# Optimization experiments

Hardware: AMD Instinct MI355X
Metric: run time of the kernel (lower is better)

Reference implementation:

```python
import jax, jax.numpy as jnp
import numpy as np
from jax import lax

B, N, DDESC = 8, 256, 128
COST_KP = 1.0
COST_DESC = 1.0
BLOCK = 128  # row block for L1 cdist


def setup_inputs() -> dict:
    key = jax.random.key(0)
    k1, k2, k3, k4, k5 = jax.random.split(key, 5)
    W, H = 640, 480
    wh = jnp.array([W, H], jnp.float32)
    kp1 = jax.random.uniform(k1, (B, N, 2)) * wh          # pixel coords
    kp2 = jax.random.uniform(k2, (B, N, 2)) * wh
    desc1 = jax.random.normal(k3, (B, N, DDESC))
    desc2 = jax.random.normal(k4, (B, N, DDESC))
    theta = jax.random.uniform(k5, (1,)) * (2.0 * jnp.pi)
    return {
        "theta": theta,
        "my_feature": jnp.concatenate([kp1, desc1], -1),
        "my_tf_feature": jnp.concatenate([kp2, desc2], -1),
        "my_width": W,
        "my_height": H,
    }


def _fundamental_8point(p1, p2):
    """Normalized 8-point algorithm (cv2.FM_8POINT): p2^T F p1 = 0, F[2,2]=1."""
    def norm(p):
        m = p.mean(0)
        d = jnp.sqrt(((p - m) ** 2).sum(1)).mean()
        s = jnp.sqrt(2.0) / d
        T = jnp.array([[1.0, 0.0, 0.0], [0.0, 1.0, 0.0], [0.0, 0.0, 0.0]]) * s \
            + jnp.zeros((3, 3)).at[0, 2].set(-s * m[0]).at[1, 2].set(-s * m[1]).at[2, 2].set(1.0)
        return (p - m) * s, T
    x1, T1 = norm(p1)
    x2, T2 = norm(p2)
    u1, v1 = x1[:, 0], x1[:, 1]
    u2, v2 = x2[:, 0], x2[:, 1]
    A = jnp.stack([u2 * u1, u2 * v1, u2, v2 * u1, v2 * v1, v2, u1, v1, jnp.ones_like(u1)], 1)
    _, _, Vt = jnp.linalg.svd(A, full_matrices=False)      # Vt: [9,9]
    Fm = Vt[-1].reshape(3, 3)
    U, S, Vt2 = jnp.linalg.svd(Fm)
    Fm = (U * S.at[2].set(0.0)) @ Vt2                      # enforce rank 2
    Fm = T2.T @ Fm @ T1
    return Fm / Fm[2, 2]


def _cdist_l1(a, b):
    """torch.cdist(p=1) without materializing [M,M,D]; blocked over rows."""
    M, D = a.shape
    ab = a.reshape(M // BLOCK, BLOCK, D)
    rows = lax.map(lambda blk: jnp.abs(blk[:, None, :] - b[None, :, :]).sum(-1), ab)
    return rows.reshape(M, b.shape[0])


def _cost_matrix(theta, my_feature, my_tf_feature, W, H):
    my_kp = my_feature[..., :2]
    my_tf_kp = my_tf_feature[..., :2]
    my_desc = my_feature[..., 2:]
    my_tf_desc = my_tf_feature[..., 2:]

    c, s = jnp.cos(theta[0]), jnp.sin(theta[0])
    zero = jnp.zeros(())
    one = jnp.ones(())
    Tm = jnp.stack([
        jnp.stack([c, -s, zero, zero]),
        jnp.stack([s, c, zero, zero]),
        jnp.stack([zero, zero, one, zero]),
        jnp.stack([zero, zero, zero, one]),
    ])  # make_transformation_M(theta, 0, 0): z-rotation, no translation

    # homogeneous image-centered coords: [B, 4, N]
    all_kp = jnp.stack([
        my_kp[:, :, 0] - 0.5 * W,
        -my_kp[:, :, 1] + 0.5 * H,
        jnp.zeros_like(my_kp[:, :, 0]),
        jnp.ones_like(my_kp[:, :, 0]),
    ], 1)
    cal = jnp.round(jnp.einsum('ij,bjn->bin', Tm, all_kp))[:, :2, :]  # [B,2,N]
    g = cal.transpose(0, 2, 1)                                        # [B,N,2]
    o = jnp.stack([g[..., 0] + 0.5 * W, -g[..., 1] + 0.5 * H], -1)    # back to pixels

    pts1 = my_tf_kp.astype(jnp.int32).reshape(B * N, 2).astype(jnp.float32)
    pts2 = o.astype(jnp.int32).reshape(B * N, 2).astype(jnp.float32)
    F = _fundamental_8point(pts1, pts2)

    ones = jnp.ones((B * N, 1), jnp.float32)
    p1h = jnp.concatenate([pts1, ones], 1)
    p2h = jnp.concatenate([pts2, ones], 1)
    cost_kp = jnp.abs((p1h @ F.astype(jnp.float32)) @ p2h.T)          # [BN, BN]

    cost_desc = _cdist_l1(my_desc.reshape(B * N, -1), my_tf_desc.reshape(B * N, -1))
    C = COST_KP * cost_kp + COST_DESC * cost_desc
    return C.reshape(B, N, B * N)


def _hungarian_np(cost):
    """scipy.optimize.linear_sum_assignment (JV shortest augmenting path), numpy."""
    cost = np.asarray(cost, dtype=np.float64)
    n = cost.shape[0]
    u = np.zeros(n)
    v = np.zeros(n)
    path = np.full(n, -1, dtype=np.int64)
    col4row = np.full(n, -1, dtype=np.int64)
    row4col = np.full(n, -1, dtype=np.int64)
    for cur_row in range(n):
        shortest = np.full(n, np.inf)
        remaining = np.ones(n, dtype=bool)
        SR = []
        i = cur_row
        min_val = 0.0
        sink = -1
        while sink == -1:
            SR.append(i)
            idx = np.nonzero(remaining)[0]
            r = min_val + cost[i, idx] - u[i] - v[idx]
            better = r < shortest[idx]
            bidx = idx[better]
            shortest[bidx] = r[better]
            path[bidx] = i
            jpos = idx[np.argmin(shortest[idx])]
            min_val = shortest[jpos]
            remaining[jpos] = False
            if row4col[jpos] == -1:
                sink = jpos
            else:
                i = row4col[jpos]
        u[cur_row] += min_val
        for i2 in SR:
            if i2 != cur_row:
                u[i2] += min_val - shortest[col4row[i2]]
        scanned = ~remaining
        v[scanned] -= min_val - shortest[scanned]
        j = sink
        while True:
            i2 = path[j]
            row4col[j] = i2
            col4row[i2], j = j, col4row[i2]
            if i2 == cur_row:
                break
    return col4row


def reference(theta, my_feature, my_tf_feature, my_width, my_height):
    C = _cost_matrix(theta, my_feature, my_tf_feature, float(my_width), float(my_height))
    Cn = np.asarray(jax.device_get(C))
    # diagonal [N,N] blocks: C.split(num_kp, -1) -> c[i] in the torch code
    cols = np.stack([_hungarian_np(Cn[i, :, i * N:(i + 1) * N]) for i in range(B)])
    rows = np.tile(np.arange(N), (B, 1))
    matches = jnp.asarray(np.stack([rows, cols], 1), dtype=jnp.int32)  # [B,2,N]
    return C, matches
```

## Files before the change

### kernel.cpp

```cpp
#include <hip/hip_runtime.h>
#include <hip/hip_bf16.h>
#include <cfloat>
#include <math.h>

#define BB 8
#define NN 256
#define BN 2048
#define DD 128
#define FEAT 130

__global__ __launch_bounds__(256) void prep_kernel(
    const float* __restrict__ theta,
    const float* __restrict__ feat1,
    const float* __restrict__ feat2,
    const int* __restrict__ wp, const int* __restrict__ hp,
    float* __restrict__ pts1, float* __restrict__ pts2) {
  int i = blockIdx.x * 256 + threadIdx.x;
  if (i >= BN) return;
  double W = (double)wp[0], H = (double)hp[0];
  double th = (double)theta[0];
  double c = cos(th), s = sin(th);
  double kx = (double)feat1[(size_t)i * FEAT + 0];
  double ky = (double)feat1[(size_t)i * FEAT + 1];
  double x = kx - 0.5 * W;
  double y = -ky + 0.5 * H;
  double calx = rint(c * x - s * y);
  double caly = rint(s * x + c * y);
  double ox = calx + 0.5 * W;
  double oy = -caly + 0.5 * H;
  pts2[2 * i]     = (float)(int)ox;
  pts2[2 * i + 1] = (float)(int)oy;
  pts1[2 * i]     = (float)(int)feat2[(size_t)i * FEAT + 0];
  pts1[2 * i + 1] = (float)(int)feat2[(size_t)i * FEAT + 1];
}

__device__ inline double wred(double x) {
#pragma unroll
  for (int off = 32; off > 0; off >>= 1) x += __shfl_down(x, off, 64);
  return x;
}

#define JROT(P, Q) {                                                          \
  double app_ = __shfl(Bc[P], P);                                             \
  double aqq_ = __shfl(Bc[Q], Q);                                             \
  double apq_ = __shfl(Bc[P], Q);                                             \
  double c_, s_;                                                              \
  if (fabs(apq_) > 1e-300) {                                                  \
    double tau_ = (aqq_ - app_) / (2.0 * apq_);                               \
    double t_ = (tau_ >= 0.0 ? 1.0 : -1.0) / (fabs(tau_) + sqrt(1.0 + tau_ * tau_)); \
    c_ = 1.0 / sqrt(1.0 + t_ * t_);                                           \
    s_ = t_ * c_;                                                             \
  } else { c_ = 1.0; s_ = 0.0; }                                              \
  const int prt_ = (jln == P) ? Q : ((jln == Q) ? P : jln);                   \
  const bool isP_ = (jln == P), isQ_ = (jln == Q);                            \
  _Pragma("unroll")                                                           \
  for (int ii = 0; ii < 9; ++ii) {                                            \
    double ob_ = __shfl(Bc[ii], prt_);                                        \
    double ov_ = __shfl(Vc[ii], prt_);                                        \
    if (isP_) { Bc[ii] = c_ * Bc[ii] - s_ * ob_; Vc[ii] = c_ * Vc[ii] - s_ * ov_; } \
    if (isQ_) { Bc[ii] = s_ * ob_ + c_ * Bc[ii]; Vc[ii] = s_ * ov_ + c_ * Vc[ii]; } \
  }                                                                           \
  { double rp_ = Bc[P], rq_ = Bc[Q];                                          \
    Bc[P] = c_ * rp_ - s_ * rq_; Bc[Q] = s_ * rp_ + c_ * rq_; } }

#define ROT3(P, Q) {                                                          \
  double apq_ = A3[P][Q];                                                     \
  double c_, s_;                                                              \
  if (fabs(apq_) > 1e-300) {                                                  \
    double tau_ = (A3[Q][Q] - A3[P][P]) / (2.0 * apq_);                       \
    double t_ = (tau_ >= 0.0 ? 1.0 : -1.0) / (fabs(tau_) + sqrt(1.0 + tau_ * tau_)); \
    c_ = 1.0 / sqrt(1.0 + t_ * t_); s_ = t_ * c_;                             \
  } else { c_ = 1.0; s_ = 0.0; }                                              \
  _Pragma("unroll")                                                           \
  for (int ii = 0; ii < 3; ++ii) { double a_ = A3[ii][P], b_ = A3[ii][Q];     \
    A3[ii][P] = c_ * a_ - s_ * b_; A3[ii][Q] = s_ * a_ + c_ * b_; }           \
  _Pragma("unroll")                                                           \
  for (int ii = 0; ii < 3; ++ii) { double a_ = A3[P][ii], b_ = A3[Q][ii];     \
    A3[P][ii] = c_ * a_ - s_ * b_; A3[Q][ii] = s_ * a_ + c_ * b_; }           \
  _Pragma("unroll")                                                           \
  for (int ii = 0; ii < 3; ++ii) { double a_ = V3[ii][P], b_ = V3[ii][Q];     \
    V3[ii][P] = c_ * a_ - s_ * b_; V3[ii][Q] = s_ * a_ + c_ * b_; } }

__global__ __launch_bounds__(256) void fmat_kernel(
    const float* __restrict__ pts1f, const float* __restrict__ pts2f,
    double* __restrict__ Fout) {
  __shared__ double sred[6];
  __shared__ double sATA[45];
  __shared__ double sV[9][16];
  __shared__ double sEv[16];
  const int tid = threadIdx.x;
  const int lane = tid & 63;
  if (tid < 6) sred[tid] = 0.0;
  if (tid < 45) sATA[tid] = 0.0;
  __syncthreads();

  double sx1 = 0, sy1 = 0, sx2 = 0, sy2 = 0;
  for (int p = tid; p < BN; p += 256) {
    sx1 += (double)pts1f[2 * p];     sy1 += (double)pts1f[2 * p + 1];
    sx2 += (double)pts2f[2 * p];     sy2 += (double)pts2f[2 * p + 1];
  }
  sx1 = wred(sx1); sy1 = wred(sy1); sx2 = wred(sx2); sy2 = wred(sy2);
  if (lane == 0) {
    atomicAdd(&sred[0], sx1); atomicAdd(&sred[1], sy1);
    atomicAdd(&sred[2], sx2); atomicAdd(&sred[3], sy2);
  }
  __syncthreads();
  const double m1x = sred[0] * (1.0 / BN), m1y = sred[1] * (1.0 / BN);
  const double m2x = sred[2] * (1.0 / BN), m2y = sred[3] * (1.0 / BN);

  double d1 = 0, d2 = 0;
  for (int p = tid; p < BN; p += 256) {
    double ax = (double)pts1f[2 * p] - m1x, ay = (double)pts1f[2 * p + 1] - m1y;
    double bx = (double)pts2f[2 * p] - m2x, by = (double)pts2f[2 * p + 1] - m2y;
    d1 += sqrt(ax * ax + ay * ay);
    d2 += sqrt(bx * bx + by * by);
  }
  d1 = wred(d1); d2 = wred(d2);
  if (lane == 0) { atomicAdd(&sred[4], d1); atomicAdd(&sred[5], d2); }
  __syncthreads();
  const double s1 = sqrt(2.0) / (sred[4] * (1.0 / BN));
  const double s2 = sqrt(2.0) / (sred[5] * (1.0 / BN));

  double acc45[45];
#pragma unroll
  for (int e = 0; e < 45; ++e) acc45[e] = 0.0;
  for (int p = tid; p < BN; p += 256) {
    double u1 = ((double)pts1f[2 * p]     - m1x) * s1;
    double v1 = ((double)pts1f[2 * p + 1] - m1y) * s1;
    double u2 = ((double)pts2f[2 * p]     - m2x) * s2;
    double v2 = ((double)pts2f[2 * p + 1] - m2y) * s2;
    double r[9] = {u2 * u1, u2 * v1, u2, v2 * u1, v2 * v1, v2, u1, v1, 1.0};
#pragma unroll
    for (int a = 0; a < 9; ++a)
#pragma unroll
      for (int b = a; b < 9; ++b)
        acc45[9 * a - (a * (a - 1)) / 2 + (b - a)] += r[a] * r[b];
  }
#pragma unroll
  for (int e = 0; e < 45; ++e) {
    double vv = wred(acc45[e]);
    if (lane == 0) atomicAdd(&sATA[e], vv);
  }
  __syncthreads();

  if (tid < 64) {
    const int jln = tid;
    double Bc[9], Vc[9];
#pragma unroll
    for (int i2 = 0; i2 < 9; ++i2) {
      if (jln < 9) {
        int a = i2 < jln ? i2 : jln;
        int b = i2 < jln ? jln : i2;
        Bc[i2] = sATA[9 * a - (a * (a - 1)) / 2 + (b - a)];
      } else Bc[i2] = 0.0;
      Vc[i2] = (i2 == jln) ? 1.0 : 0.0;
    }
    for (int sw = 0; sw < 7; ++sw) {
      JROT(0,1) JROT(0,2) JROT(0,3) JROT(0,4) JROT(0,5) JROT(0,6) JROT(0,7) JROT(0,8)
      JROT(1,2) JROT(1,3) JROT(1,4) JROT(1,5) JROT(1,6) JROT(1,7) JROT(1,8)
      JROT(2,3) JROT(2,4) JROT(2,5) JROT(2,6) JROT(2,7) JROT(2,8)
      JROT(3,4) JROT(3,5) JROT(3,6) JROT(3,7) JROT(3,8)
      JROT(4,5) JROT(4,6) JROT(4,7) JROT(4,8)
      JROT(5,6) JROT(5,7) JROT(5,8)
      JROT(6,7) JROT(6,8)
      JROT(7,8)
    }
    double ev = 0.0;
#pragma unroll
    for (int i2 = 0; i2 < 9; ++i2) if (jln == i2) ev = Bc[i2];
    if (jln < 9) {
      sEv[jln] = ev;
#pragma unroll
      for (int i2 = 0; i2 < 9; ++i2) sV[i2][jln] = Vc[i2];
    }
  }
  __syncthreads();

  if (tid == 0) {
    int jm = 0; double be = sEv[0];
#pragma unroll
    for (int jj = 1; jj < 9; ++jj) if (sEv[jj] < be) { be = sEv[jj]; jm = jj; }
    double F0[9];
#pragma unroll
    for (int i2 = 0; i2 < 9; ++i2) F0[i2] = sV[i2][jm];
    double M00 = F0[0], M01 = F0[1], M02 = F0[2];
    double M10 = F0[3], M11 = F0[4], M12 = F0[5];
    double M20 = F0[6], M21 = F0[7], M22 = F0[8];
    double A3[3][3], V3[3][3];
    A3[0][0] = M00*M00 + M10*M10 + M20*M20;
    A3[0][1] = M00*M01 + M10*M11 + M20*M21;
    A3[0][2] = M00*M02 + M10*M12 + M20*M22;
    A3[1][1] = M01*M01 + M11*M11 + M21*M21;
    A3[1][2] = M01*M02 + M11*M12 + M21*M22;
    A3[2][2] = M02*M02 + M12*M12 + M22*M22;
    A3[1][0] = A3[0][1]; A3[2][0] = A3[0][2]; A3[2][1] = A3[1][2];
#pragma unroll
    for (int ii = 0; ii < 3; ++ii)
#pragma unroll
      for (int jj = 0; jj < 3; ++jj) V3[ii][jj] = (ii == jj) ? 1.0 : 0.0;
    for (int sw = 0; sw < 10; ++sw) { ROT3(0,1) ROT3(0,2) ROT3(1,2) }
    double w0 = A3[0][0], w1 = A3[1][1], w2 = A3[2][2];
    double vx, vy, vz;
    if (w0 <= w1 && w0 <= w2)      { vx = V3[0][0]; vy = V3[1][0]; vz = V3[2][0]; }
    else if (w1 <= w2)             { vx = V3[0][1]; vy = V3[1][1]; vz = V3[2][1]; }
    else                           { vx = V3[0][2]; vy = V3[1][2]; vz = V3[2][2]; }
    double Mv0 = M00 * vx + M01 * vy + M02 * vz;
    double Mv1 = M10 * vx + M11 * vy + M12 * vz;
    double Mv2 = M20 * vx + M21 * vy + M22 * vz;
    double F200 = M00 - Mv0 * vx, F201 = M01 - Mv0 * vy, F202 = M02 - Mv0 * vz;
    double F210 = M10 - Mv1 * vx, F211 = M11 - Mv1 * vy, F212 = M12 - Mv1 * vz;
    double F220 = M20 - Mv2 * vx, F221 = M21 - Mv2 * vy, F222 = M22 - Mv2 * vz;
    double R00 = s2 * F200, R01 = s2 * F201, R02 = s2 * F202;
    double R10 = s2 * F210, R11 = s2 * F211, R12 = s2 * F212;
    double R20 = -s2 * m2x * F200 - s2 * m2y * F210 + F220;
    double R21 = -s2 * m2x * F201 - s2 * m2y * F211 + F221;
    double R22 = -s2 * m2x * F202 - s2 * m2y * F212 + F222;
    double D00 = s1 * R00, D10 = s1 * R10, D20 = s1 * R20;
    double D01 = s1 * R01, D11 = s1 * R11, D21 = s1 * R21;
    double D02 = -s1 * m1x * R00 - s1 * m1y * R01 + R02;
    double D12 = -s1 * m1x * R10 - s1 * m1y * R11 + R12;
    double D22 = -s1 * m1x * R20 - s1 * m1y * R21 + R22;
    Fout[0] = D00 / D22; Fout[1] = D01 / D22; Fout[2] = D02 / D22;
    Fout[3] = D10 / D22; Fout[4] = D11 / D22; Fout[5] = D12 / D22;
    Fout[6] = D20 / D22; Fout[7] = D21 / D22; Fout[8] = D22 / D22;
  }
}

__global__ __launch_bounds__(256) void cost_kernel(
    const float* __restrict__ feat1,
    const float* __restrict__ feat2,
    const float* __restrict__ pts1,
    const float* __restrict__ pts2,
    const double* __restrict__ Fd,
    float* __restrict__ Cout) {
  __shared__ float D1[128][68];
  __shared__ float D2[128][68];
  __shared__ float a0s[64], a1s[64], a2s[64], p2xs[64], p2ys[64];
  const int tid = threadIdx.x;
  const int rowbase = blockIdx.y * 64;
  const int colbase = blockIdx.x * 64;
#pragma unroll
  for (int it = 0; it < 32; ++it) {
    int idx = it * 256 + tid;
    int r = idx >> 7, k = idx & 127;
    D1[k][r] = feat1[(size_t)(rowbase + r) * FEAT + 2 + k];
    D2[k][r] = feat2[(size_t)(colbase + r) * FEAT + 2 + k];
  }
  if (tid < 64) {
    float x1 = pts1[2 * (rowbase + tid)], y1 = pts1[2 * (rowbase + tid) + 1];
    a0s[tid] = (float)(Fd[0] * x1 + Fd[3] * y1 + Fd[6]);
    a1s[tid] = (float)(Fd[1] * x1 + Fd[4] * y1 + Fd[7]);
    a2s[tid] = (float)(Fd[2] * x1 + Fd[5] * y1 + Fd[8]);
    p2xs[tid] = pts2[2 * (colbase + tid)];
    p2ys[tid] = pts2[2 * (colbase + tid) + 1];
  }
  __syncthreads();
  const int tx = tid & 15, ty = tid >> 4;
  float acc[4][4] = {};
#pragma unroll 4
  for (int k = 0; k < 128; ++k) {
    float4 av = *(const float4*)&D1[k][ty * 4];
    float4 bv = *(const float4*)&D2[k][tx * 4];
    float ar[4] = {av.x, av.y, av.z, av.w};
    float br[4] = {bv.x, bv.y, bv.z, bv.w};
#pragma unroll
    for (int r = 0; r < 4; ++r)
#pragma unroll
      for (int c = 0; c < 4; ++c)
        acc[r][c] += fabsf(ar[r] - br[c]);
  }
#pragma unroll
  for (int r = 0; r < 4; ++r) {
    int row = rowbase + ty * 4 + r;
    float a0 = a0s[ty * 4 + r], a1 = a1s[ty * 4 + r], a2 = a2s[ty * 4 + r];
    float4 o;
    float* op = &o.x;
#pragma unroll
    for (int c = 0; c < 4; ++c) {
      float kp = fabsf(a0 * p2xs[tx * 4 + c] + a1 * p2ys[tx * 4 + c] + a2);
      op[c] = acc[r][c] + kp;
    }
    *(float4*)&Cout[(size_t)row * BN + colbase + tx * 4] = o;
  }
}

#define NROWS_C 152

__device__ __forceinline__ unsigned long long sortkey(double d) {
  long long b = __double_as_longlong(d);
  long long m = (b >> 63) | (long long)0x8000000000000000LL;
  return (unsigned long long)(b ^ m);
}

template<int CTRL>
__device__ __forceinline__ unsigned dpprm32(unsigned x) {
  int y = __builtin_amdgcn_update_dpp(0, (int)x, CTRL, 0xF, 0xF, true);
  unsigned u = (unsigned)y;
  return u < x ? u : x;
}
template<int CTRL>
__device__ __forceinline__ unsigned long long dpprm64(unsigned long long x) {
  int lo = (int)(unsigned)x, hi = (int)(unsigned)(x >> 32);
  int lo2 = __builtin_amdgcn_update_dpp(0, lo, CTRL, 0xF, 0xF, true);
  int hi2 = __builtin_amdgcn_update_dpp(0, hi, CTRL, 0xF, 0xF, true);
  unsigned long long y =
      ((unsigned long long)(unsigned)hi2 << 32) | (unsigned)lo2;
  return y < x ? y : x;
}

__device__ __forceinline__ unsigned wave_min_u32(unsigned x) {
  unsigned h = dpprm32<0x121>(x);
  h = dpprm32<0x122>(h);
  h = dpprm32<0x124>(h);
  h = dpprm32<0x128>(h);
  unsigned g0 = (unsigned)__builtin_amdgcn_readlane((int)h, 0);
  unsigned g1 = (unsigned)__builtin_amdgcn_readlane((int)h, 16);
  unsigned g2 = (unsigned)__builtin_amdgcn_readlane((int)h, 32);
  unsigned g3 = (unsigned)__builtin_amdgcn_readlane((int)h, 48);
  unsigned ga = g0 < g1 ? g0 : g1, gb = g2 < g3 ? g2 : g3;
  return ga < gb ? ga : gb;
}

__device__ __forceinline__ double rl64(double x, int l) {
  long long bb = __double_as_longlong(x);
  int lo = __builtin_amdgcn_readlane((int)(bb & 0xFFFFFFFFLL), l);
  int hi = __builtin_amdgcn_readlane((int)(bb >> 32), l);
  return __longlong_as_double(((long long)hi << 32) | (unsigned)lo);
}
__device__ __forceinline__ unsigned long long rdpair(unsigned ghi, unsigned glo, int l) {
  return ((unsigned long long)(unsigned)__builtin_amdgcn_readlane((int)ghi, l) << 32)
       | (unsigned)__builtin_amdgcn_readlane((int)glo, l);
}

#define UPD(K, CK, KK, SH, PP) {                                       \
  double d_ = (base + (double)(CK)) - v##K;                            \
  bool a_ = ((rem >> (K)) & 1u) && (d_ < (SH));                        \
  (SH) = a_ ? d_ : (SH);                                               \
  (KK) = a_ ? sortkey(d_) : (KK);                                      \
  (PP) = a_ ? i : (PP); }

#define ROWLOAD(I) ((I) < NROWS_C ? *(const float4*)&rcache[(I)][lane * 4]   \
                                  : *(const float4*)(Cb + (size_t)(I) * BN + lane * 4))

#define R4C_OF(LI) ((LI) == 0 ? r4c0 : (LI) == 1 ? r4c1 : (LI) == 2 ? r4c2 : r4c3)
#define U4_OF(LI)  ((LI) == 0 ? u40  : (LI) == 1 ? u41  : (LI) == 2 ? u42  : u43)
#define SH_OF(LI)  ((LI) == 0 ? sh0  : (LI) == 1 ? sh1  : (LI) == 2 ? sh2  : sh3)

__global__ __launch_bounds__(64) void hungarian_kernel(
    const float* __restrict__ C, float* __restrict__ out_matches) {
  const int b = blockIdx.x;
  const int lane = threadIdx.x;
  __shared__ float rcache[NROWS_C][NN];
  __shared__ int c4r_lds[NN];
  __shared__ double u_sd[NN];
  __shared__ int flist[NN];
  const float* Cb = C + (size_t)b * NN * BN + (size_t)b * NN;

  for (int t = lane; t < NROWS_C * (NN / 4); t += 64) {
    int r = t >> 6, q = t & 63;
    *(float4*)&rcache[r][q * 4] = *(const float4*)(Cb + (size_t)r * BN + q * 4);
  }
  for (int r = lane; r < NN; r += 64) c4r_lds[r] = -1;
  __syncthreads();

  for (int i = 0; i < NN; ++i) {
    float4 cr = ROWLOAD(i);
    float m01 = fminf(cr.x, cr.y), m23 = fminf(cr.z, cr.w);
    unsigned gm = wave_min_u32(__float_as_uint(fminf(m01, m23)));
    if (lane == 0) u_sd[i] = (double)__uint_as_float(gm);
  }
  __syncthreads();

  double v0, v1, v2, v3;
  int am0 = 0, am1 = 0, am2 = 0, am3 = 0;
  {
    double c0 = DBL_MAX, c1 = DBL_MAX, c2 = DBL_MAX, c3 = DBL_MAX;
    for (int i = 0; i < NN; ++i) {
      float4 cr = ROWLOAD(i);
      double uu = u_sd[i];
      double s0 = (double)cr.x - uu; if (s0 < c0) { c0 = s0; am0 = i; }
      double s1 = (double)cr.y - uu; if (s1 < c1) { c1 = s1; am1 = i; }
      double s2 = (double)cr.z - uu; if (s2 < c2) { c2 = s2; am2 = i; }
      double s3 = (double)cr.w - uu; if (s3 < c3) { c3 = s3; am3 = i; }
    }
    v0 = c0; v1 = c1; v2 = c2; v3 = c3;
  }

  int r4c0, r4c1, r4c2, r4c3;
  { int old = atomicCAS(&c4r_lds[am0], -1, lane * 4 + 0); r4c0 = (old == -1) ? am0 : -1; }
  { int old = atomicCAS(&c4r_lds[am1], -1, lane * 4 + 1); r4c1 = (old == -1) ? am1 : -1; }
  { int old = atomicCAS(&c4r_lds[am2], -1, lane * 4 + 2); r4c2 = (old == -1) ? am2 : -1; }
  { int old = atomicCAS(&c4r_lds[am3], -1, lane * 4 + 3); r4c3 = (old == -1) ? am3 : -1; }
  __syncthreads();
  int c4r0 = c4r_lds[lane * 4 + 0];
  int c4r1 = c4r_lds[lane * 4 + 1];
  int c4r2 = c4r_lds[lane * 4 + 2];
  int c4r3 = c4r_lds[lane * 4 + 3];
  double u40 = (r4c0 >= 0) ? u_sd[r4c0] : 0.0;
  double u41 = (r4c1 >= 0) ? u_sd[r4c1] : 0.0;
  double u42 = (r4c2 >= 0) ? u_sd[r4c2] : 0.0;
  double u43 = (r4c3 >= 0) ? u_sd[r4c3] : 0.0;

  int totfree = 0;
  for (int r0 = 0; r0 < NN; r0 += 64) {
    bool fr = (c4r_lds[r0 + lane] < 0);
    unsigned long long mask = __ballot(fr);
    int idx = totfree + __builtin_popcountll(mask & ((1ULL << lane) - 1ULL));
    if (fr) flist[idx] = r0 + lane;
    totfree += (int)__builtin_popcountll(mask);
  }
  __syncthreads();

  const unsigned long long KMAX = 0xFFFFFFFFFFFFFFFFULL;

  for (int fi = 0; fi < totfree; ++fi) {
    const int cur = flist[fi];
    unsigned long long k0 = KMAX, k1 = KMAX, k2 = KMAX, k3 = KMAX;
    double sh0 = DBL_MAX, sh1 = DBL_MAX, sh2 = DBL_MAX, sh3 = DBL_MAX;
    int p0 = -1, p1 = -1, p2 = -1, p3 = -1;
    unsigned rem = 0xFu;
    double minval = 0.0;
    const double ucur0 = u_sd[cur];
    double ui = ucur0;
    int i = cur;
    int sink = -1;
    float4 cr = ROWLOAD(cur);
    while (true) {
      double base = minval - ui;
      UPD(0, cr.x, k0, sh0, p0)
      UPD(1, cr.y, k1, sh1, p1)
      UPD(2, cr.z, k2, sh2, p2)
      UPD(3, cr.w, k3, sh3, p3)
      unsigned long long m01 = k0 < k1 ? k0 : k1;
      unsigned long long m23 = k2 < k3 ? k2 : k3;
      unsigned long long kl = m01 < m23 ? m01 : m23;
      int myli = (k0 == kl) ? 0 : (k1 == kl) ? 1 : (k2 == kl) ? 2 : 3;
      double mysh = SH_OF(myli);
      double myu  = U4_OF(myli);
      int myrc    = R4C_OF(myli);
      unsigned packed = ((unsigned)(myrc + 1) & 0xFFFFu) | ((unsigned)myli << 16);
      unsigned hi = (unsigned)(kl >> 32);
      unsigned mh = wave_min_u32(hi);
      unsigned long long bal = __ballot(hi == mh);
      int wl;
      if (__builtin_popcountll(bal) == 1) {
        wl = (int)__builtin_ctzll(bal);
      } else {
        unsigned long long gg = dpprm64<0x121>(kl);
        gg = dpprm64<0x122>(gg); gg = dpprm64<0x124>(gg); gg = dpprm64<0x128>(gg);
        unsigned glo2 = (unsigned)gg, ghi2 = (unsigned)(gg >> 32);
        unsigned long long r0 = rdpair(ghi2, glo2, 0);
        unsigned long long r1 = rdpair(ghi2, glo2, 16);
        unsigned long long r2 = rdpair(ghi2, glo2, 32);
        unsigned long long r3 = rdpair(ghi2, glo2, 48);
        unsigned long long ra = r0 < r1 ? r0 : r1, rb = r2 < r3 ? r2 : r3;
        unsigned long long g = ra < rb ? ra : rb;
        bal = __ballot(kl == g);
        wl = (int)__builtin_ctzll(bal);
      }
      int pk = __builtin_amdgcn_readlane((int)packed, wl);
      minval = rl64(mysh, wl);
      double uin = rl64(myu, wl);
      int rc = (pk & 0xFFFF) - 1;
      int li = pk >> 16;
      float4 nxt;
      if (rc >= 0) nxt = ROWLOAD(rc);
      if (lane == wl) {
        if (myli == 0)      k0 = KMAX;
        else if (myli == 1) k1 = KMAX;
        else if (myli == 2) k2 = KMAX;
        else                k3 = KMAX;
        rem &= ~(1u << myli);
      }
      if (rc < 0) { sink = wl * 4 + li; break; }
      ui = uin;
      i = rc;
      cr = nxt;
    }
    if (!(rem & 1u)) { double dl = minval - sh0; v0 -= dl; if (r4c0 >= 0) u40 += dl; }
    if (!(rem & 2u)) { double dl = minval - sh1; v1 -= dl; if (r4c1 >= 0) u41 += dl; }
    if (!(rem & 4u)) { double dl = minval - sh2; v2 -= dl; if (r4c2 >= 0) u42 += dl; }
    if (!(rem & 8u)) { double dl = minval - sh3; v3 -= dl; if (r4c3 >= 0) u43 += dl; }
    int j = sink;
    while (true) {
      int slot = j & 3, ow = j >> 2;
      int myp = (slot == 0) ? p0 : (slot == 1) ? p1 : (slot == 2) ? p2 : p3;
      int i2 = __builtin_amdgcn_readlane(myp, ow);
      int s2 = i2 & 3, ow2 = i2 >> 2;
      int myc = (s2 == 0) ? c4r0 : (s2 == 1) ? c4r1 : (s2 == 2) ? c4r2 : c4r3;
      int jn = __builtin_amdgcn_readlane(myc, ow2);
      double newu;
      if (i2 == cur) {
        newu = ucur0 + minval;
      } else {
        int slj = jn & 3, owj = jn >> 2;
        double myuj = (slj == 0) ? u40 : (slj == 1) ? u41
                    : (slj == 2) ? u42 : u43;
        newu = rl64(myuj, owj);
      }
      if (lane == ow) {
        if (slot == 0) { r4c0 = i2; u40 = newu; }
        else if (slot == 1) { r4c1 = i2; u41 = newu; }
        else if (slot == 2) { r4c2 = i2; u42 = newu; }
        else { r4c3 = i2; u43 = newu; }
      }
      if (lane == ow2) {
        if (s2 == 0) c4r0 = j; else if (s2 == 1) c4r1 = j;
        else if (s2 == 2) c4r2 = j; else c4r3 = j;
      }
      if (i2 == cur) break;
      j = jn;
    }
  }

  float4 ridx, cidx;
  ridx.x = (float)(lane * 4 + 0); ridx.y = (float)(lane * 4 + 1);
  ridx.z = (float)(lane * 4 + 2); ridx.w = (float)(lane * 4 + 3);
  cidx.x = (float)c4r0; cidx.y = (float)c4r1;
  cidx.z = (float)c4r2; cidx.w = (float)c4r3;
  *(float4*)&out_matches[b * 2 * NN + lane * 4] = ridx;
  *(float4*)&out_matches[b * 2 * NN + NN + lane * 4] = cidx;
}

extern "C" void kernel_launch(void* const* d_in, const int* in_sizes, int n_in,
                              void* d_out, int out_size, void* d_ws, size_t ws_size,
                              hipStream_t stream) {
  const float* theta = (const float*)d_in[0];
  const float* feat1 = (const float*)d_in[1];
  const float* feat2 = (const float*)d_in[2];
  const int* wp = (const int*)d_in[3];
  const int* hp = (const int*)d_in[4];
  float* out = (float*)d_out;

  float* pts1 = (float*)d_ws;
  float* pts2 = pts1 + 2 * BN;
  double* Fd = (double*)(pts2 + 2 * BN);

  prep_kernel<<<BN / 256, 256, 0, stream>>>(theta, feat1, feat2, wp, hp, pts1, pts2);
  fmat_kernel<<<1, 256, 0, stream>>>(pts1, pts2, Fd);
  dim3 grid(BN / 64, BN / 64);
  cost_kernel<<<grid, 256, 0, stream>>>(feat1, feat2, pts1, pts2, Fd, out);
  hungarian_kernel<<<BB, 64, 0, stream>>>(out, out + (size_t)BN * BN);
}
```

Baseline: 1.733 ms.

## Fuse prep into fmat kernel, cut Jacobi sweeps, simplify Hungarian min keys

```diff
diff --git a/kernel.cpp b/kernel.cpp
--- a/kernel.cpp
+++ b/kernel.cpp
@@ -8,31 +8,6 @@
 #define BN 2048
 #define DD 128
 #define FEAT 130
-
-__global__ __launch_bounds__(256) void prep_kernel(
-    const float* __restrict__ theta,
-    const float* __restrict__ feat1,
-    const float* __restrict__ feat2,
-    const int* __restrict__ wp, const int* __restrict__ hp,
-    float* __restrict__ pts1, float* __restrict__ pts2) {
-  int i = blockIdx.x * 256 + threadIdx.x;
-  if (i >= BN) return;
-  double W = (double)wp[0], H = (double)hp[0];
-  double th = (double)theta[0];
-  double c = cos(th), s = sin(th);
-  double kx = (double)feat1[(size_t)i * FEAT + 0];
-  double ky = (double)feat1[(size_t)i * FEAT + 1];
-  double x = kx - 0.5 * W;
-  double y = -ky + 0.5 * H;
-  double calx = rint(c * x - s * y);
-  double caly = rint(s * x + c * y);
-  double ox = calx + 0.5 * W;
-  double oy = -caly + 0.5 * H;
-  pts2[2 * i]     = (float)(int)ox;
-  pts2[2 * i + 1] = (float)(int)oy;
-  pts1[2 * i]     = (float)(int)feat2[(size_t)i * FEAT + 0];
-  pts1[2 * i + 1] = (float)(int)feat2[(size_t)i * FEAT + 1];
-}
 
 __device__ inline double wred(double x) {
 #pragma unroll
@@ -82,7 +57,11 @@
     V3[ii][P] = c_ * a_ - s_ * b_; V3[ii][Q] = s_ * a_ + c_ * b_; } }
 
 __global__ __launch_bounds__(256) void fmat_kernel(
-    const float* __restrict__ pts1f, const float* __restrict__ pts2f,
+    const float* __restrict__ theta,
+    const float* __restrict__ feat1,
+    const float* __restrict__ feat2,
+    const int* __restrict__ wp, const int* __restrict__ hp,
+    float* pts1f, float* pts2f,
     double* __restrict__ Fout) {
   __shared__ double sred[6];
   __shared__ double sATA[45];
@@ -92,6 +71,26 @@
   const int lane = tid & 63;
   if (tid < 6) sred[tid] = 0.0;
   if (tid < 45) sATA[tid] = 0.0;
+
+  {
+    double W = (double)wp[0], H = (double)hp[0];
+    double th = (double)theta[0];
+    double c = cos(th), s = sin(th);
+    for (int i = tid; i < BN; i += 256) {
+      double kx = (double)feat1[(size_t)i * FEAT + 0];
+      double ky = (double)feat1[(size_t)i * FEAT + 1];
+      double x = kx - 0.5 * W;
+      double y = -ky + 0.5 * H;
+      double calx = rint(c * x - s * y);
+      double caly = rint(s * x + c * y);
+      double ox = calx + 0.5 * W;
+      double oy = -caly + 0.5 * H;
+      pts2f[2 * i]     = (float)(int)ox;
+      pts2f[2 * i + 1] = (float)(int)oy;
+      pts1f[2 * i]     = (float)(int)feat2[(size_t)i * FEAT + 0];
+      pts1f[2 * i + 1] = (float)(int)feat2[(size_t)i * FEAT + 1];
+    }
+  }
   __syncthreads();
 
   double sx1 = 0, sy1 = 0, sx2 = 0, sy2 = 0;
@@ -155,7 +154,7 @@
       } else Bc[i2] = 0.0;
       Vc[i2] = (i2 == jln) ? 1.0 : 0.0;
     }
-    for (int sw = 0; sw < 7; ++sw) {
+    for (int sw = 0; sw < 5; ++sw) {
       JROT(0,1) JROT(0,2) JROT(0,3) JROT(0,4) JROT(0,5) JROT(0,6) JROT(0,7) JROT(0,8)
       JROT(1,2) JROT(1,3) JROT(1,4) JROT(1,5) JROT(1,6) JROT(1,7) JROT(1,8)
       JROT(2,3) JROT(2,4) JROT(2,5) JROT(2,6) JROT(2,7) JROT(2,8)
@@ -284,13 +283,7 @@
   }
 }
 
-#define NROWS_C 152
-
-__device__ __forceinline__ unsigned long long sortkey(double d) {
-  long long b = __double_as_longlong(d);
-  long long m = (b >> 63) | (long long)0x8000000000000000LL;
-  return (unsigned long long)(b ^ m);
-}
+#define NROWS_C 153
 
 template<int CTRL>
 __device__ __forceinline__ unsigned dpprm32(unsigned x) {
@@ -332,11 +325,10 @@
        | (unsigned)__builtin_amdgcn_readlane((int)glo, l);
 }
 
-#define UPD(K, CK, KK, SH, PP) {                                       \
+#define UPD(K, CK, SH, PP) {                                           \
   double d_ = (base + (double)(CK)) - v##K;                            \
   bool a_ = ((rem >> (K)) & 1u) && (d_ < (SH));                        \
   (SH) = a_ ? d_ : (SH);                                               \
-  (KK) = a_ ? sortkey(d_) : (KK);                                      \
   (PP) = a_ ? i : (PP); }
 
 #define ROWLOAD(I) ((I) < NROWS_C ? *(const float4*)&rcache[(I)][lane * 4]   \
@@ -353,7 +345,6 @@
   __shared__ float rcache[NROWS_C][NN];
   __shared__ int c4r_lds[NN];
   __shared__ double u_sd[NN];
-  __shared__ int flist[NN];
   const float* Cb = C + (size_t)b * NN * BN + (size_t)b * NN;
 
   for (int t = lane; t < NROWS_C * (NN / 4); t += 64) {
@@ -401,6 +392,7 @@
   double u42 = (r4c2 >= 0) ? u_sd[r4c2] : 0.0;
   double u43 = (r4c3 >= 0) ? u_sd[r4c3] : 0.0;
 
+  int* flist = c4r_lds;
   int totfree = 0;
   for (int r0 = 0; r0 < NN; r0 += 64) {
     bool fr = (c4r_lds[r0 + lane] < 0);
@@ -411,11 +403,10 @@
   }
   __syncthreads();
 
-  const unsigned long long KMAX = 0xFFFFFFFFFFFFFFFFULL;
+  const unsigned long long INF64 = 0x7FF0000000000000ULL;
 
   for (int fi = 0; fi < totfree; ++fi) {
     const int cur = flist[fi];
-    unsigned long long k0 = KMAX, k1 = KMAX, k2 = KMAX, k3 = KMAX;
     double sh0 = DBL_MAX, sh1 = DBL_MAX, sh2 = DBL_MAX, sh3 = DBL_MAX;
     int p0 = -1, p1 = -1, p2 = -1, p3 = -1;
     unsigned rem = 0xFu;
@@ -427,14 +418,18 @@
     float4 cr = ROWLOAD(cur);
     while (true) {
       double base = minval - ui;
-      UPD(0, cr.x, k0, sh0, p0)
-      UPD(1, cr.y, k1, sh1, p1)
-      UPD(2, cr.z, k2, sh2, p2)
-      UPD(3, cr.w, k3, sh3, p3)
-      unsigned long long m01 = k0 < k1 ? k0 : k1;
-      unsigned long long m23 = k2 < k3 ? k2 : k3;
+      UPD(0, cr.x, sh0, p0)
+      UPD(1, cr.y, sh1, p1)
+      UPD(2, cr.z, sh2, p2)
+      UPD(3, cr.w, sh3, p3)
+      unsigned long long b0 = (rem & 1u) ? (unsigned long long)__double_as_longlong(sh0) : INF64;
+      unsigned long long b1 = (rem & 2u) ? (unsigned long long)__double_as_longlong(sh1) : INF64;
+      unsigned long long b2 = (rem & 4u) ? (unsigned long long)__double_as_longlong(sh2) : INF64;
+      unsigned long long b3 = (rem & 8u) ? (unsigned long long)__double_as_longlong(sh3) : INF64;
+      unsigned long long m01 = b0 < b1 ? b0 : b1;
+      unsigned long long m23 = b2 < b3 ? b2 : b3;
       unsigned long long kl = m01 < m23 ? m01 : m23;
-      int myli = (k0 == kl) ? 0 : (k1 == kl) ? 1 : (k2 == kl) ? 2 : 3;
+      int myli = (b0 == kl) ? 0 : (b1 == kl) ? 1 : (b2 == kl) ? 2 : 3;
       double mysh = SH_OF(myli);
       double myu  = U4_OF(myli);
       int myrc    = R4C_OF(myli);
@@ -465,13 +460,7 @@
       int li = pk >> 16;
       float4 nxt;
       if (rc >= 0) nxt = ROWLOAD(rc);
-      if (lane == wl) {
-        if (myli == 0)      k0 = KMAX;
-        else if (myli == 1) k1 = KMAX;
-        else if (myli == 2) k2 = KMAX;
-        else                k3 = KMAX;
-        rem &= ~(1u << myli);
-      }
+      if (lane == wl) rem &= ~(1u << myli);
       if (rc < 0) { sink = wl * 4 + li; break; }
       ui = uin;
       i = rc;
@@ -536,8 +525,7 @@
   float* pts2 = pts1 + 2 * BN;
   double* Fd = (double*)(pts2 + 2 * BN);
 
-  prep_kernel<<<BN / 256, 256, 0, stream>>>(theta, feat1, feat2, wp, hp, pts1, pts2);
-  fmat_kernel<<<1, 256, 0, stream>>>(pts1, pts2, Fd);
+  fmat_kernel<<<1, 256, 0, stream>>>(theta, feat1, feat2, wp, hp, pts1, pts2, Fd);
   dim3 grid(BN / 64, BN / 64);
   cost_kernel<<<grid, 256, 0, stream>>>(feat1, feat2, pts1, pts2, Fd, out);
   hungarian_kernel<<<BB, 64, 0, stream>>>(out, out + (size_t)BN * BN);
```

After: 1.684 ms. 1.03x faster.
